# Kernel optimization log

Measured on AMD Instinct MI355X. Metric: run time of the kernel, lower is better.

Reference implementation:

```python
import jax, jax.numpy as jnp
import numpy as np

B, CIN, COUT, K = 4096, 128, 128, 9  # batch, in_ch, out_ch, board size / n_offsets


def setup_inputs() -> dict:
    key = jax.random.key(0)
    k1, k2, k3 = jax.random.split(key, 3)
    inputs = jax.random.normal(k1, (B, CIN, K, K), dtype=jnp.float32)   # [B, Cin, 9, 9]
    weights = jax.random.normal(k2, (K, COUT, CIN), dtype=jnp.float32)  # per-offset linear
    bias = jax.random.normal(k3, (K, COUT), dtype=jnp.float32)
    return {"inputs": inputs, "weights": weights, "bias": bias}


def reference(inputs, weights, bias):
    # For each vertical offset k (row of the 9x9 board), gather the slice
    # inputs[:, :, k, :] and apply the k-th linear map plus its bias.
    # out[b, k, oc, x] = sum_i W[k, oc, i] * inputs[b, i, k, x] + bias[k, oc]
    out = jnp.einsum('bikx,koi->bkox', inputs, weights)  # [B, 9, Cout, 9]
    out = out + bias[None, :, :, None]
    return out
```

## Files before the change

kernel.cpp:

```cpp
#include <hip/hip_runtime.h>
#include <hip/hip_bf16.h>


#define NB   4096
#define CINC 128
#define COUTC 128
#define NK   9
#define NX   9
#define BT   16
#define NCOL (BT * NX)
#define LDK  136

typedef __attribute__((ext_vector_type(8))) short short8;
typedef __attribute__((ext_vector_type(4))) float floatx4;

__device__ __forceinline__ short f2bf(float f) {
    union { float f; unsigned u; } v; v.f = f;
    unsigned r = v.u + 0x7fff + ((v.u >> 16) & 1);
    return (short)(r >> 16);
}

__global__ __launch_bounds__(512, 6) void GatherVertical_40656160424516_kernel(
    const float* __restrict__ in, const float* __restrict__ w,
    const float* __restrict__ bias, float* __restrict__ out)
{
    __shared__ short Il[NCOL * LDK];

    const int t = threadIdx.x;

    const int j = blockIdx.x;
    const int xcd = j & 7;
    const int slot = j >> 3;
    const int grp = slot / 9;
    const int k = slot - grp * 9;
    const int btile = grp * 8 + xcd;
    const int b0 = btile * BT;

    const int lane = t & 63;
    const int wv = t >> 6;
    const int lc = lane & 15;
    const int quad = lane >> 4;
    const int oc_base = wv * 16;

    const float* wk = w + k * (COUTC * CINC);
    short8 afr[4];
    #pragma unroll
    for (int s = 0; s < 4; ++s) {
        const float* wp = wk + (oc_base + lc) * CINC + s * 32 + quad * 8;
        float4 w0 = *(const float4*)wp;
        float4 w1 = *(const float4*)(wp + 4);
        short8 a;
        a[0] = f2bf(w0.x); a[1] = f2bf(w0.y); a[2] = f2bf(w0.z); a[3] = f2bf(w0.w);
        a[4] = f2bf(w1.x); a[5] = f2bf(w1.y); a[6] = f2bf(w1.z); a[7] = f2bf(w1.w);
        afr[s] = a;
    }

    const float* bk = bias + k * COUTC;
    float bsv[4];
    #pragma unroll
    for (int r = 0; r < 4; ++r) bsv[r] = bk[oc_base + quad * 4 + r];

    const float* inb = in + (size_t)b0 * (CINC * NK * NX) + k * NX;
    #pragma unroll
    for (int it = 0; it < 36; ++it) {
        int f = it * 512 + t;
        int bl = f / (CINC * NX);
        int rem = f - bl * (CINC * NX);
        int i = rem / NX;
        int x = rem - i * NX;
        float v = inb[bl * (CINC * NK * NX) + i * (NK * NX) + x];
        Il[(bl * NX + x) * LDK + i] = f2bf(v);
    }

    __syncthreads();

    floatx4 acc[9];
    #pragma unroll
    for (int n = 0; n < 9; ++n) acc[n] = (floatx4){0.f, 0.f, 0.f, 0.f};

    #pragma unroll
    for (int s = 0; s < 4; ++s) {
        int kof = s * 32 + quad * 8;
        #pragma unroll
        for (int n = 0; n < 9; ++n) {
            short8 bfr = *(const short8*)&Il[(n * 16 + lc) * LDK + kof];
            acc[n] = __builtin_amdgcn_mfma_f32_16x16x32_bf16(afr[s], bfr, acc[n], 0, 0, 0);
        }
    }

    #pragma unroll
    for (int n = 0; n < 9; ++n) {
        int nx = n * 16 + lc;
        int bl = nx / 9;
        int x = nx - bl * 9;
        float* op = out + (size_t)(b0 + bl) * (NK * COUTC * NX) + k * (COUTC * NX)
                        + (oc_base + quad * 4) * NX + x;
        #pragma unroll
        for (int r = 0; r < 4; ++r)
            op[r * NX] = acc[n][r] + bsv[r];
    }
}

extern "C" void kernel_launch(void* const* d_in, const int* in_sizes, int n_in,
                              void* d_out, int out_size, void* d_ws, size_t ws_size,
                              hipStream_t stream) {
    const float* in  = (const float*)d_in[0];
    const float* w   = (const float*)d_in[1];
    const float* bs  = (const float*)d_in[2];
    float* out = (float*)d_out;
    dim3 grid((NB / BT) * NK);
    dim3 block(512);
    GatherVertical_40656160424516_kernel<<<grid, block, 0, stream>>>(in, w, bs, out);
}
```

Baseline: 352.3 us.

## Loop over all offsets per block with contiguous input rows and LDS-staged coalesced stores

Each block now handles two batch items across all nine offsets instead of sixteen batches for one offset. Each input row is read contiguously with vector loads, where before the per-offset slices were strided gathers. Outputs are staged through LDS and written as float4 coalesced stores. Weights and bias for the next offset are prefetched in registers during the current MFMA step. The tradeoffs are reloading weights from L2 for every block, extra syncthreads per offset, and far less MFMA work per block.

New measurement: 437.8 us. +24.3%, slower.

```diff
diff --git a/kernel.cpp b/kernel.cpp
--- a/kernel.cpp
+++ b/kernel.cpp
@@ -2,17 +2,22 @@
 #include <hip/hip_bf16.h>
 
 
-#define NB   4096
-#define CINC 128
+#define NB    4096
+#define CINC  128
 #define COUTC 128
-#define NK   9
-#define NX   9
-#define BT   16
-#define NCOL (BT * NX)
-#define LDK  136
+#define NK    9
+#define NX    9
+#define BT    2
+#define ROWF  (NK * NX)
+#define LDK   136
+#define KSTR  (18 * LDK)
+#define OUTK  (COUTC * NX)
+#define OUTB  (NK * COUTC * NX)
 
 typedef __attribute__((ext_vector_type(8))) short short8;
 typedef __attribute__((ext_vector_type(4))) float floatx4;
+
+struct F4 { float x, y, z, w; };
 
 __device__ __forceinline__ short f2bf(float f) {
     union { float f; unsigned u; } v; v.f = f;
@@ -20,21 +25,34 @@
     return (short)(r >> 16);
 }
 
+__device__ __forceinline__ constexpr int koff(int kx) {
+    return (kx / 9) * KSTR + (kx % 9) * LDK;
+}
+
+template<int KX0>
+__device__ __forceinline__ void stage20(short* lb, const float* p) {
+    F4 v[5];
+    #pragma unroll
+    for (int c = 0; c < 5; ++c) v[c] = *(const F4*)(p + 4 * c);
+    #pragma unroll
+    for (int c = 0; c < 5; ++c) {
+        lb[koff(KX0 + 4 * c + 0)] = f2bf(v[c].x);
+        lb[koff(KX0 + 4 * c + 1)] = f2bf(v[c].y);
+        lb[koff(KX0 + 4 * c + 2)] = f2bf(v[c].z);
+        lb[koff(KX0 + 4 * c + 3)] = f2bf(v[c].w);
+    }
+}
+
 __global__ __launch_bounds__(512, 6) void GatherVertical_40656160424516_kernel(
     const float* __restrict__ in, const float* __restrict__ w,
     const float* __restrict__ bias, float* __restrict__ out)
 {
-    __shared__ short Il[NCOL * LDK];
+    __shared__ __align__(16) char smem[9 * KSTR * 2 + BT * OUTK * 4];
+    short* Il = (short*)smem;
+    float* Ol = (float*)(smem + 9 * KSTR * 2);
 
     const int t = threadIdx.x;
-
-    const int j = blockIdx.x;
-    const int xcd = j & 7;
-    const int slot = j >> 3;
-    const int grp = slot / 9;
-    const int k = slot - grp * 9;
-    const int btile = grp * 8 + xcd;
-    const int b0 = btile * BT;
+    const int b0 = blockIdx.x * BT;
 
     const int lane = t & 63;
     const int wv = t >> 6;
@@ -42,62 +60,91 @@
     const int quad = lane >> 4;
     const int oc_base = wv * 16;
 
-    const float* wk = w + k * (COUTC * CINC);
-    short8 afr[4];
-    #pragma unroll
-    for (int s = 0; s < 4; ++s) {
-        const float* wp = wk + (oc_base + lc) * CINC + s * 32 + quad * 8;
-        float4 w0 = *(const float4*)wp;
-        float4 w1 = *(const float4*)(wp + 4);
-        short8 a;
-        a[0] = f2bf(w0.x); a[1] = f2bf(w0.y); a[2] = f2bf(w0.z); a[3] = f2bf(w0.w);
-        a[4] = f2bf(w1.x); a[5] = f2bf(w1.y); a[6] = f2bf(w1.z); a[7] = f2bf(w1.w);
-        afr[s] = a;
+    const int r = t & 255;
+    const int h = t >> 8;
+    const int bb = r >> 7;
+    const int i = r & 127;
+
+    const float* rowp = in + ((size_t)(b0 + bb) * CINC + i) * ROWF + 40 * h;
+    short* lb = Il + bb * (NX * LDK) + i;
+
+    if (h == 0) {
+        stage20<0>(lb, rowp);
+        stage20<20>(lb, rowp + 20);
+    } else {
+        stage20<40>(lb, rowp);
+        stage20<60>(lb, rowp + 20);
+        lb[koff(80)] = f2bf(rowp[40]);
     }
 
-    const float* bk = bias + k * COUTC;
-    float bsv[4];
-    #pragma unroll
-    for (int r = 0; r < 4; ++r) bsv[r] = bk[oc_base + quad * 4 + r];
-
-    const float* inb = in + (size_t)b0 * (CINC * NK * NX) + k * NX;
-    #pragma unroll
-    for (int it = 0; it < 36; ++it) {
-        int f = it * 512 + t;
-        int bl = f / (CINC * NX);
-        int rem = f - bl * (CINC * NX);
-        int i = rem / NX;
-        int x = rem - i * NX;
-        float v = inb[bl * (CINC * NK * NX) + i * (NK * NX) + x];
-        Il[(bl * NX + x) * LDK + i] = f2bf(v);
-    }
+    short8 afrA[4], afrB[4];
+    float bsA[4], bsB[4];
+    auto loadWB = [&](int k, short8* afr, float* bs) {
+        const float* wp = w + k * (COUTC * CINC) + (oc_base + lc) * CINC + quad * 8;
+        #pragma unroll
+        for (int s = 0; s < 4; ++s) {
+            float4 w0 = *(const float4*)(wp + s * 32);
+            float4 w1 = *(const float4*)(wp + s * 32 + 4);
+            short8 a;
+            a[0] = f2bf(w0.x); a[1] = f2bf(w0.y); a[2] = f2bf(w0.z); a[3] = f2bf(w0.w);
+            a[4] = f2bf(w1.x); a[5] = f2bf(w1.y); a[6] = f2bf(w1.z); a[7] = f2bf(w1.w);
+            afr[s] = a;
+        }
+        const float* bp = bias + k * COUTC + oc_base + quad * 4;
+        #pragma unroll
+        for (int rr = 0; rr < 4; ++rr) bs[rr] = bp[rr];
+    };
+    loadWB(0, afrA, bsA);
 
     __syncthreads();
 
-    floatx4 acc[9];
-    #pragma unroll
-    for (int n = 0; n < 9; ++n) acc[n] = (floatx4){0.f, 0.f, 0.f, 0.f};
+    for (int k = 0; k < NK; ++k) {
+        if (k < NK - 1) loadWB(k + 1, afrB, bsB);
 
-    #pragma unroll
-    for (int s = 0; s < 4; ++s) {
-        int kof = s * 32 + quad * 8;
+        floatx4 acc0 = {0.f, 0.f, 0.f, 0.f};
+        floatx4 acc1 = {0.f, 0.f, 0.f, 0.f};
+        const short* bp = Il + k * KSTR + lc * LDK + quad * 8;
         #pragma unroll
-        for (int n = 0; n < 9; ++n) {
-            short8 bfr = *(const short8*)&Il[(n * 16 + lc) * LDK + kof];
-            acc[n] = __builtin_amdgcn_mfma_f32_16x16x32_bf16(afr[s], bfr, acc[n], 0, 0, 0);
+        for (int s = 0; s < 4; ++s) {
+            short8 bf0 = *(const short8*)(bp + s * 32);
+            short8 bf1 = *(const short8*)(bp + 16 * LDK + s * 32);
+            acc0 = __builtin_amdgcn_mfma_f32_16x16x32_bf16(afrA[s], bf0, acc0, 0, 0, 0);
+            acc1 = __builtin_amdgcn_mfma_f32_16x16x32_bf16(afrA[s], bf1, acc1, 0, 0, 0);
         }
-    }
 
-    #pragma unroll
-    for (int n = 0; n < 9; ++n) {
-        int nx = n * 16 + lc;
-        int bl = nx / 9;
-        int x = nx - bl * 9;
-        float* op = out + (size_t)(b0 + bl) * (NK * COUTC * NX) + k * (COUTC * NX)
-                        + (oc_base + quad * 4) * NX + x;
+        if (k > 0) __syncthreads();
+
+        {
+            int bcp = lc >= 9;
+            int x = lc - bcp * 9;
+            float* op = Ol + (bcp * COUTC + oc_base + quad * 4) * NX + x;
+            #pragma unroll
+            for (int rr = 0; rr < 4; ++rr) op[rr * NX] = acc0[rr] + bsA[rr];
+            if (lc < 2) {
+                float* op1 = Ol + (COUTC + oc_base + quad * 4) * NX + 7 + lc;
+                #pragma unroll
+                for (int rr = 0; rr < 4; ++rr) op1[rr * NX] = acc1[rr] + bsA[rr];
+            }
+        }
+        __syncthreads();
+
+        {
+            float* dstb = out + (size_t)b0 * OUTB + k * OUTK;
+            int bcp = t >= 288;
+            int off = (t - bcp * 288) * 4;
+            floatx4 v = *(const floatx4*)(Ol + bcp * OUTK + off);
+            *(floatx4*)(dstb + bcp * OUTB + off) = v;
+            if (t < 64) {
+                int off2 = (224 + t) * 4;
+                floatx4 v2 = *(const floatx4*)(Ol + OUTK + off2);
+                *(floatx4*)(dstb + OUTB + off2) = v2;
+            }
+        }
+
         #pragma unroll
-        for (int r = 0; r < 4; ++r)
-            op[r * NX] = acc[n][r] + bsv[r];
+        for (int s = 0; s < 4; ++s) afrA[s] = afrB[s];
+        #pragma unroll
+        for (int rr = 0; rr < 4; ++rr) bsA[rr] = bsB[rr];
     }
 }
 
@@ -108,7 +155,7 @@
     const float* w   = (const float*)d_in[1];
     const float* bs  = (const float*)d_in[2];
     float* out = (float*)d_out;
-    dim3 grid((NB / BT) * NK);
+    dim3 grid(NB / BT);
     dim3 block(512);
     GatherVertical_40656160424516_kernel<<<grid, block, 0, stream>>>(in, w, bs, out);
 }
```
